# Kernel tuning notes

Hardware: AMD Instinct MI355X
Metric: run time of the kernel (lower is better)

The kernel has to match this reference:

```python
import jax, jax.numpy as jnp
import numpy as np
from jax import lax

N = 8388608
NG = 1024
TAU = 0.1
GAMMA = 0.05
MAX_ITERS = 30
EPS = 1e-9


def setup_inputs() -> dict:
    key = jax.random.key(0)
    k1, k2, k3 = jax.random.split(key, 3)
    y_raw = jax.random.uniform(k1, (N,), dtype=jnp.float32)
    y_real = jax.random.uniform(k2, (N,), dtype=jnp.float32)
    group_ids = jax.random.randint(k3, (N,), 0, NG, dtype=jnp.int32)
    return {"y_raw": y_raw, "y_real": y_real, "group_ids": group_ids, "n_groups": NG}


def reference(y_raw, y_real, group_ids, n_groups):
    y_real = jnp.maximum(y_real, EPS)
    l = (1.0 - TAU) * y_real          # per-element lower box bound
    u = (1.0 + TAU) * y_real          # per-element upper box bound
    y_clipped = jnp.clip(y_raw, l, u)
    w = 1.0 / jnp.maximum(y_real, 1e-9)

    seg_sum = lambda v: jax.ops.segment_sum(v, group_ids, num_segments=n_groups)

    n_g = seg_sum(jnp.ones_like(y_raw))            # [G] group sizes
    L = (1.0 - GAMMA) * n_g
    U = (1.0 + GAMMA) * n_g
    S0 = seg_sum(w * y_clipped)                    # [G] ratio sums at alpha=0
    feasible = (S0 >= L) & (S0 <= U)

    # per-group bracketing interval for alpha
    alo = jax.ops.segment_min((l - y_raw) * w, group_ids, num_segments=n_groups) - 1.0
    ahi = jax.ops.segment_max((u - y_raw) * w, group_ids, num_segments=n_groups) + 1.0
    nonempty = n_g > 0
    alo = jnp.where(nonempty, alo, 0.0)            # guard empty groups (inf/-inf)
    ahi = jnp.where(nonempty, ahi, 0.0)
    T = jnp.where(S0 < L, L, U)                    # [G] bisection target

    def step(carry, _):
        lo, hi, _ = carry
        mid = 0.5 * (lo + hi)                                    # [G]
        y_mid = jnp.clip(y_raw + mid[group_ids] / w, l, u)       # [N]
        Smid = seg_sum(w * y_mid)                                # [G]
        lo = jnp.where(Smid < T, mid, lo)
        hi = jnp.where(Smid >= T, mid, hi)
        return (lo, hi, mid), None

    (lo, hi, mid), _ = lax.scan(step, (alo, ahi, alo), None, length=MAX_ITERS)
    y_bis = jnp.clip(y_raw + mid[group_ids] / w, l, u)           # last iterate y_mid
    return jnp.where(feasible[group_ids], y_clipped, y_bis)
```

## Files before the change

kernel.cpp:

```cpp
#include <hip/hip_runtime.h>

#define NGROUPS  1024
#define EPSF     1e-9f
#define MAX_ITERS 30
#define SUM_MASK ((1ull << 49) - 1)
#define CNT_SHIFT 49
#define FIX_SCALE 1073741824.0f
#define FIX_INV   (1.0 / 1073741824.0)
#define SBLK 512
#define STILE 4

__device__ __forceinline__ unsigned enc_f(float f) {
    unsigned u = __float_as_uint(f);
    return (u & 0x80000000u) ? ~u : (u | 0x80000000u);
}
__device__ __forceinline__ float dec_f(unsigned e) {
    unsigned u = (e & 0x80000000u) ? (e ^ 0x80000000u) : ~e;
    return __uint_as_float(u);
}

__global__ __launch_bounds__(NGROUPS) void k_init(unsigned long long* gpack) {
    gpack[threadIdx.x] = 0ull;
}

template <bool EXACT>
__global__ __launch_bounds__(SBLK, 2) void k_stats(const float4* __restrict__ yraw4,
                                                   const float4* __restrict__ yreal4,
                                                   const int4*   __restrict__ gid4,
                                                   float4*       __restrict__ out4,
                                                   unsigned long long* gpack, int n4) {
    __shared__ unsigned long long s_pk[NGROUPS];
    int t = threadIdx.x;
    s_pk[t] = 0ull; s_pk[t + SBLK] = 0ull;
    __syncthreads();

    int base = blockIdx.x * (SBLK * STILE) + t;
    if (EXACT) {
        float4 yr[STILE], ye[STILE];
        int4   gg[STILE];
#pragma unroll
        for (int k = 0; k < STILE; ++k) yr[k] = yraw4[base + k * SBLK];
#pragma unroll
        for (int k = 0; k < STILE; ++k) ye[k] = yreal4[base + k * SBLK];
#pragma unroll
        for (int k = 0; k < STILE; ++k) gg[k] = gid4[base + k * SBLK];
#pragma unroll
        for (int k = 0; k < STILE; ++k) {
            float yrs[4] = { yr[k].x, yr[k].y, yr[k].z, yr[k].w };
            float yes[4] = { ye[k].x, ye[k].y, ye[k].z, ye[k].w };
            int   gs[4]  = { gg[k].x, gg[k].y, gg[k].z, gg[k].w };
            float oc[4];
#pragma unroll
            for (int j = 0; j < 4; ++j) {
                float yraw = yrs[j];
                float yrc  = fmaxf(yes[j], EPSF);
                float l = 0.9f * yrc;
                float u = 1.1f * yrc;
                float yclip = fminf(fmaxf(yraw, l), u);
                oc[j] = yclip;
                float s = yclip / yrc;
                unsigned long long pk = (1ull << CNT_SHIFT)
                    + (unsigned long long)__float2uint_rn(s * FIX_SCALE);
                atomicAdd(&s_pk[gs[j]], pk);
            }
            out4[base + k * SBLK] = make_float4(oc[0], oc[1], oc[2], oc[3]);
        }
    } else {
#pragma unroll
        for (int k = 0; k < STILE; ++k) {
            int i = base + k * SBLK;
            if (i >= n4) continue;
            float4 a = yraw4[i], b = yreal4[i];
            int4 g4 = gid4[i];
            float yrs[4] = { a.x, a.y, a.z, a.w };
            float yes[4] = { b.x, b.y, b.z, b.w };
            int   gs[4]  = { g4.x, g4.y, g4.z, g4.w };
            float oc[4];
#pragma unroll
            for (int j = 0; j < 4; ++j) {
                float yrc  = fmaxf(yes[j], EPSF);
                float l = 0.9f * yrc, u = 1.1f * yrc;
                float yclip = fminf(fmaxf(yrs[j], l), u);
                oc[j] = yclip;
                unsigned long long pk = (1ull << CNT_SHIFT)
                    + (unsigned long long)__float2uint_rn((yclip / yrc) * FIX_SCALE);
                atomicAdd(&s_pk[gs[j]], pk);
            }
            out4[i] = make_float4(oc[0], oc[1], oc[2], oc[3]);
        }
    }
    __syncthreads();
    unsigned long long v0 = s_pk[t], v1 = s_pk[t + SBLK];
    if (v0) atomicAdd(&gpack[t], v0);
    if (v1) atomicAdd(&gpack[t + SBLK], v1);
}

__global__ __launch_bounds__(NGROUPS) void k_group(const unsigned long long* gpack,
                                                   unsigned* feas, float* gT,
                                                   unsigned* gmn, unsigned* gmx,
                                                   unsigned* gbase, unsigned* gcur,
                                                   unsigned* total) {
    __shared__ unsigned s_scan[NGROUPS];
    int g = threadIdx.x;
    unsigned long long pk = gpack[g];
    unsigned c = (unsigned)(pk >> CNT_SHIFT);
    float S0 = (float)((double)(pk & SUM_MASK) * FIX_INV);
    float nf = (float)c;
    float L = 0.95f * nf;
    float U = 1.05f * nf;
    unsigned f = (S0 >= L && S0 <= U) ? 1u : 0u;
    feas[g] = f;
    gT[g]   = (S0 < L) ? L : U;
    gmn[g]  = 0xFFFFFFFFu;
    gmx[g]  = 0u;

    unsigned v = f ? 0u : c;
    s_scan[g] = v;
    for (int off = 1; off < NGROUPS; off <<= 1) {
        __syncthreads();
        unsigned tmp = (g >= off) ? s_scan[g - off] : 0u;
        __syncthreads();
        s_scan[g] += tmp;
    }
    __syncthreads();
    unsigned incl = s_scan[g];
    unsigned base = incl - v;
    gbase[g] = base;
    gcur[g]  = base;
    if (g == NGROUPS - 1) *total = incl;
}

__global__ __launch_bounds__(256) void k_mmc(const float4* __restrict__ yraw4,
                                             const float4* __restrict__ yreal4,
                                             const int4*   __restrict__ gid4,
                                             const unsigned* __restrict__ feas,
                                             unsigned* gcur, const unsigned* total,
                                             unsigned* gmn, unsigned* gmx,
                                             unsigned* cidx, unsigned* cgid,
                                             unsigned capacity, int n4) {
    if (*total == 0u) return;
    __shared__ unsigned s_feas[NGROUPS];
    __shared__ unsigned s_mn[NGROUPS];
    __shared__ unsigned s_mx[NGROUPS];
    for (int g = threadIdx.x; g < NGROUPS; g += blockDim.x) {
        s_feas[g] = feas[g]; s_mn[g] = 0xFFFFFFFFu; s_mx[g] = 0u;
    }
    __syncthreads();
    int stride = gridDim.x * blockDim.x;
    for (int i = blockIdx.x * blockDim.x + threadIdx.x; i < n4; i += stride) {
        int4 gg = gid4[i];
        int gs[4] = { gg.x, gg.y, gg.z, gg.w };
        bool any = !s_feas[gs[0]] || !s_feas[gs[1]] || !s_feas[gs[2]] || !s_feas[gs[3]];
        if (!any) continue;
        float4 yr = yraw4[i];
        float4 ye = yreal4[i];
        float yrs[4] = { yr.x, yr.y, yr.z, yr.w };
        float yes[4] = { ye.x, ye.y, ye.z, ye.w };
#pragma unroll
        for (int j = 0; j < 4; ++j) {
            int g = gs[j];
            if (s_feas[g]) continue;
            float yraw = yrs[j];
            float yrc  = fmaxf(yes[j], EPSF);
            float l = 0.9f * yrc;
            float u = 1.1f * yrc;
            float w = 1.0f / yrc;
            float a0 = (l - yraw) * w;
            float a1 = (u - yraw) * w;
            atomicMin(&s_mn[g], enc_f(a0));
            atomicMax(&s_mx[g], enc_f(a1));
            unsigned pos = atomicAdd(&gcur[g], 1u);
            if (pos < capacity) {
                cidx[pos] = (unsigned)(4 * i + j);
                cgid[pos] = (unsigned)g;
            }
        }
    }
    __syncthreads();
    for (int g = threadIdx.x; g < NGROUPS; g += blockDim.x) {
        if (!s_feas[g]) {
            atomicMin(&gmn[g], s_mn[g]);
            atomicMax(&gmx[g], s_mx[g]);
        }
    }
}

#define CAPC 8064
__global__ __launch_bounds__(256) void k_bisect(const float* __restrict__ y_raw,
                                                const float* __restrict__ y_real,
                                                const unsigned* feas,
                                                const unsigned long long* gpack,
                                                const unsigned* gbase, const float* gT,
                                                const unsigned* gmn, const unsigned* gmx,
                                                const unsigned* __restrict__ cidx,
                                                float* __restrict__ out,
                                                unsigned capacity) {
    int g = blockIdx.x;
    if (feas[g]) return;
    __shared__ float2 cache[CAPC];
    __shared__ double s_part[4];
    __shared__ float  s_mid;
    unsigned base = gbase[g];
    unsigned cnt  = (unsigned)(gpack[g] >> CNT_SHIFT);
    if (base >= capacity) cnt = 0;
    else if (cnt > capacity - base) cnt = capacity - base;
    int t = threadIdx.x;
    for (unsigned i = t; i < cnt && i < CAPC; i += 256u) {
        unsigned idx = cidx[base + i];
        cache[i] = make_float2(y_raw[idx], y_real[idx]);
    }
    __syncthreads();
    float lo = dec_f(gmn[g]) - 1.0f;
    float hi = dec_f(gmx[g]) + 1.0f;
    float T  = gT[g];
    for (int it = 0; it < MAX_ITERS; ++it) {
        if (t == 0) s_mid = 0.5f * (lo + hi);
        __syncthreads();
        float m = s_mid;
        double part = 0.0;
        for (unsigned i = t; i < cnt; i += 256u) {
            float yraw, ye;
            if (i < CAPC) { float2 v = cache[i]; yraw = v.x; ye = v.y; }
            else { unsigned idx = cidx[base + i]; yraw = y_raw[idx]; ye = y_real[idx]; }
            float yrc = fmaxf(ye, EPSF);
            float l = 0.9f * yrc;
            float u = 1.1f * yrc;
            float w = 1.0f / yrc;
            float ym = fminf(fmaxf(yraw + m / w, l), u);
            part += (double)(w * ym);
        }
#pragma unroll
        for (int off = 32; off > 0; off >>= 1) part += __shfl_down(part, off, 64);
        if ((t & 63) == 0) s_part[t >> 6] = part;
        __syncthreads();
        if (t == 0) {
            float Smid = (float)(s_part[0] + s_part[1] + s_part[2] + s_part[3]);
            if (Smid < T) lo = m; else hi = m;
        }
        __syncthreads();
    }
    float m = s_mid;
    for (unsigned i = t; i < cnt; i += 256u) {
        unsigned idx = cidx[base + i];
        float yraw, ye;
        if (i < CAPC) { float2 v = cache[i]; yraw = v.x; ye = v.y; }
        else { yraw = y_raw[idx]; ye = y_real[idx]; }
        float yrc = fmaxf(ye, EPSF);
        float l = 0.9f * yrc;
        float u = 1.1f * yrc;
        float w = 1.0f / yrc;
        out[idx] = fminf(fmaxf(yraw + m / w, l), u);
    }
}

extern "C" void kernel_launch(void* const* d_in, const int* in_sizes, int n_in,
                              void* d_out, int out_size, void* d_ws, size_t ws_size,
                              hipStream_t stream) {
    const float* y_raw  = (const float*)d_in[0];
    const float* y_real = (const float*)d_in[1];
    const int*   gid    = (const int*)d_in[2];
    float* out = (float*)d_out;
    const int n  = in_sizes[0];
    const int n4 = n / 4;

    char* ws = (char*)d_ws;
    unsigned long long* gpack = (unsigned long long*)(ws + 0);
    unsigned* gmn    = (unsigned*)(ws + 8192);
    unsigned* gmx    = (unsigned*)(ws + 12288);
    unsigned* feas   = (unsigned*)(ws + 16384);
    float*    gT     = (float*)(ws + 20480);
    unsigned* gbase  = (unsigned*)(ws + 24576);
    unsigned* gcur   = (unsigned*)(ws + 28672);
    unsigned* total  = (unsigned*)(ws + 32768);
    unsigned* cidx   = (unsigned*)(ws + 40960);
    size_t cap64 = (ws_size > 40960) ? (ws_size - 40960) / 8 : 0;
    if (cap64 > (size_t)n) cap64 = (size_t)n;
    unsigned capacity = (unsigned)cap64;
    unsigned* cgid = cidx + capacity;

    const int per_blk = SBLK * STILE;
    k_init<<<1, NGROUPS, 0, stream>>>(gpack);
    if (n4 % per_blk == 0) {
        k_stats<true><<<n4 / per_blk, SBLK, 0, stream>>>(
            (const float4*)y_raw, (const float4*)y_real, (const int4*)gid,
            (float4*)out, gpack, n4);
    } else {
        k_stats<false><<<(n4 + per_blk - 1) / per_blk, SBLK, 0, stream>>>(
            (const float4*)y_raw, (const float4*)y_real, (const int4*)gid,
            (float4*)out, gpack, n4);
    }
    k_group<<<1, NGROUPS, 0, stream>>>(gpack, feas, gT, gmn, gmx, gbase, gcur, total);
    k_mmc<<<512, 256, 0, stream>>>((const float4*)y_raw, (const float4*)y_real,
                                   (const int4*)gid, feas, gcur, total,
                                   gmn, gmx, cidx, cgid, capacity, n4);
    k_bisect<<<NGROUPS, 256, 0, stream>>>(y_raw, y_real, feas, gpack, gbase, gT,
                                          gmn, gmx, cidx, out, capacity);
}
```

Before: 148.5 us.

## Restructure stats kernel as strided software-pipelined loop and add early exits when all groups feasible

```diff
diff --git a/kernel.cpp b/kernel.cpp
--- a/kernel.cpp
+++ b/kernel.cpp
@@ -7,8 +7,9 @@
 #define CNT_SHIFT 49
 #define FIX_SCALE 1073741824.0f
 #define FIX_INV   (1.0 / 1073741824.0)
-#define SBLK 512
-#define STILE 4
+#define SBLK 256
+#define SITER 4
+#define SGRID 2048
 
 __device__ __forceinline__ unsigned enc_f(float f) {
     unsigned u = __float_as_uint(f);
@@ -23,76 +24,73 @@
     gpack[threadIdx.x] = 0ull;
 }
 
+__device__ __forceinline__ void proc_tile(const float4& a, const float4& b,
+                                          const int4& g4, float4* outp,
+                                          unsigned long long* s_pk) {
+    float yrs[4] = { a.x, a.y, a.z, a.w };
+    float yes[4] = { b.x, b.y, b.z, b.w };
+    int   gs[4]  = { g4.x, g4.y, g4.z, g4.w };
+    float oc[4];
+#pragma unroll
+    for (int j = 0; j < 4; ++j) {
+        float yraw = yrs[j];
+        float yrc  = fmaxf(yes[j], EPSF);
+        float l = 0.9f * yrc;
+        float u = 1.1f * yrc;
+        float yclip = fminf(fmaxf(yraw, l), u);
+        oc[j] = yclip;
+        float s = yclip / yrc;
+        unsigned long long pk = (1ull << CNT_SHIFT)
+            + (unsigned long long)__float2uint_rn(s * FIX_SCALE);
+        atomicAdd(&s_pk[gs[j]], pk);
+    }
+    *outp = make_float4(oc[0], oc[1], oc[2], oc[3]);
+}
+
 template <bool EXACT>
-__global__ __launch_bounds__(SBLK, 2) void k_stats(const float4* __restrict__ yraw4,
-                                                   const float4* __restrict__ yreal4,
-                                                   const int4*   __restrict__ gid4,
-                                                   float4*       __restrict__ out4,
-                                                   unsigned long long* gpack, int n4) {
+__global__ __launch_bounds__(SBLK) void k_stats(const float4* __restrict__ yraw4,
+                                                const float4* __restrict__ yreal4,
+                                                const int4*   __restrict__ gid4,
+                                                float4*       __restrict__ out4,
+                                                unsigned long long* gpack, int n4) {
     __shared__ unsigned long long s_pk[NGROUPS];
     int t = threadIdx.x;
-    s_pk[t] = 0ull; s_pk[t + SBLK] = 0ull;
-    __syncthreads();
-
-    int base = blockIdx.x * (SBLK * STILE) + t;
+#pragma unroll
+    for (int g = t; g < NGROUPS; g += SBLK) s_pk[g] = 0ull;
+    __syncthreads();
+
+    int stride = gridDim.x * SBLK;
+    int i = blockIdx.x * SBLK + t;
     if (EXACT) {
-        float4 yr[STILE], ye[STILE];
-        int4   gg[STILE];
-#pragma unroll
-        for (int k = 0; k < STILE; ++k) yr[k] = yraw4[base + k * SBLK];
-#pragma unroll
-        for (int k = 0; k < STILE; ++k) ye[k] = yreal4[base + k * SBLK];
-#pragma unroll
-        for (int k = 0; k < STILE; ++k) gg[k] = gid4[base + k * SBLK];
-#pragma unroll
-        for (int k = 0; k < STILE; ++k) {
-            float yrs[4] = { yr[k].x, yr[k].y, yr[k].z, yr[k].w };
-            float yes[4] = { ye[k].x, ye[k].y, ye[k].z, ye[k].w };
-            int   gs[4]  = { gg[k].x, gg[k].y, gg[k].z, gg[k].w };
-            float oc[4];
-#pragma unroll
-            for (int j = 0; j < 4; ++j) {
-                float yraw = yrs[j];
-                float yrc  = fmaxf(yes[j], EPSF);
-                float l = 0.9f * yrc;
-                float u = 1.1f * yrc;
-                float yclip = fminf(fmaxf(yraw, l), u);
-                oc[j] = yclip;
-                float s = yclip / yrc;
-                unsigned long long pk = (1ull << CNT_SHIFT)
-                    + (unsigned long long)__float2uint_rn(s * FIX_SCALE);
-                atomicAdd(&s_pk[gs[j]], pk);
+        float4 a = yraw4[i];
+        float4 b = yreal4[i];
+        int4   g = gid4[i];
+#pragma unroll
+        for (int k = 0; k < SITER; ++k) {
+            float4 an, bn; int4 gn;
+            if (k < SITER - 1) {
+                an = yraw4[i + stride];
+                bn = yreal4[i + stride];
+                gn = gid4[i + stride];
             }
-            out4[base + k * SBLK] = make_float4(oc[0], oc[1], oc[2], oc[3]);
+            proc_tile(a, b, g, &out4[i], s_pk);
+            i += stride;
+            a = an; b = bn; g = gn;
         }
     } else {
-#pragma unroll
-        for (int k = 0; k < STILE; ++k) {
-            int i = base + k * SBLK;
-            if (i >= n4) continue;
-            float4 a = yraw4[i], b = yreal4[i];
-            int4 g4 = gid4[i];
-            float yrs[4] = { a.x, a.y, a.z, a.w };
-            float yes[4] = { b.x, b.y, b.z, b.w };
-            int   gs[4]  = { g4.x, g4.y, g4.z, g4.w };
-            float oc[4];
-#pragma unroll
-            for (int j = 0; j < 4; ++j) {
-                float yrc  = fmaxf(yes[j], EPSF);
-                float l = 0.9f * yrc, u = 1.1f * yrc;
-                float yclip = fminf(fmaxf(yrs[j], l), u);
-                oc[j] = yclip;
-                unsigned long long pk = (1ull << CNT_SHIFT)
-                    + (unsigned long long)__float2uint_rn((yclip / yrc) * FIX_SCALE);
-                atomicAdd(&s_pk[gs[j]], pk);
-            }
-            out4[i] = make_float4(oc[0], oc[1], oc[2], oc[3]);
-        }
-    }
-    __syncthreads();
-    unsigned long long v0 = s_pk[t], v1 = s_pk[t + SBLK];
-    if (v0) atomicAdd(&gpack[t], v0);
-    if (v1) atomicAdd(&gpack[t + SBLK], v1);
+        for (; i < n4; i += stride) {
+            float4 a = yraw4[i];
+            float4 b = yreal4[i];
+            int4   g = gid4[i];
+            proc_tile(a, b, g, &out4[i], s_pk);
+        }
+    }
+    __syncthreads();
+#pragma unroll
+    for (int g = t; g < NGROUPS; g += SBLK) {
+        unsigned long long v = s_pk[g];
+        if (v) atomicAdd(&gpack[g], v);
+    }
 }
 
 __global__ __launch_bounds__(NGROUPS) void k_group(const unsigned long long* gpack,
@@ -101,7 +99,10 @@
                                                    unsigned* gbase, unsigned* gcur,
                                                    unsigned* total) {
     __shared__ unsigned s_scan[NGROUPS];
+    __shared__ unsigned s_any;
     int g = threadIdx.x;
+    if (g == 0) s_any = 0u;
+    __syncthreads();
     unsigned long long pk = gpack[g];
     unsigned c = (unsigned)(pk >> CNT_SHIFT);
     float S0 = (float)((double)(pk & SUM_MASK) * FIX_INV);
@@ -113,9 +114,14 @@
     gT[g]   = (S0 < L) ? L : U;
     gmn[g]  = 0xFFFFFFFFu;
     gmx[g]  = 0u;
-
     unsigned v = f ? 0u : c;
     s_scan[g] = v;
+    if (!f) atomicOr(&s_any, 1u);
+    __syncthreads();
+    if (s_any == 0u) {
+        if (g == 0) *total = 0u;
+        return;
+    }
     for (int off = 1; off < NGROUPS; off <<= 1) {
         __syncthreads();
         unsigned tmp = (g >= off) ? s_scan[g - off] : 0u;
@@ -193,8 +199,10 @@
                                                 const unsigned* gbase, const float* gT,
                                                 const unsigned* gmn, const unsigned* gmx,
                                                 const unsigned* __restrict__ cidx,
+                                                const unsigned* total,
                                                 float* __restrict__ out,
                                                 unsigned capacity) {
+    if (*total == 0u) return;
     int g = blockIdx.x;
     if (feas[g]) return;
     __shared__ float2 cache[CAPC];
@@ -278,14 +286,15 @@
     unsigned capacity = (unsigned)cap64;
     unsigned* cgid = cidx + capacity;
 
-    const int per_blk = SBLK * STILE;
     k_init<<<1, NGROUPS, 0, stream>>>(gpack);
-    if (n4 % per_blk == 0) {
-        k_stats<true><<<n4 / per_blk, SBLK, 0, stream>>>(
+    const int tiles_total = SGRID * SBLK * SITER;
+    if (n4 == tiles_total) {
+        k_stats<true><<<SGRID, SBLK, 0, stream>>>(
             (const float4*)y_raw, (const float4*)y_real, (const int4*)gid,
             (float4*)out, gpack, n4);
     } else {
-        k_stats<false><<<(n4 + per_blk - 1) / per_blk, SBLK, 0, stream>>>(
+        int nb = (n4 + SBLK * SITER - 1) / (SBLK * SITER);
+        k_stats<false><<<nb, SBLK, 0, stream>>>(
             (const float4*)y_raw, (const float4*)y_real, (const int4*)gid,
             (float4*)out, gpack, n4);
     }
@@ -294,5 +303,5 @@
                                    (const int4*)gid, feas, gcur, total,
                                    gmn, gmx, cidx, cgid, capacity, n4);
     k_bisect<<<NGROUPS, 256, 0, stream>>>(y_raw, y_real, feas, gpack, gbase, gT,
-                                          gmn, gmx, cidx, out, capacity);
-}
+                                          gmn, gmx, cidx, total, out, capacity);
+}
```

New measurement: 167.2 us. 1.13x slower.
